# Performance work log

Measured on AMD Instinct MI355X. Metric: run time of the kernel, lower is better.

Reference implementation:

```python
import jax, jax.numpy as jnp
import numpy as np

ANGSTROM2BOHR = 1.8897261258369282
CUTOFF_ANGSTROM = 5.2  # module's `cutoff` init arg, converted to bohr in forward


def smooth_cutoff(d, rc):
    # torchani 'smooth' cutoff: exp(1 - 1/(1 - (d/rc)^2)) for d < rc, else 0
    x2 = (d / rc) ** 2
    x2_safe = jnp.where(x2 < 1.0, x2, 0.0)  # avoid inf inside the masked branch
    return jnp.where(d < rc, jnp.exp(1.0 - 1.0 / (1.0 - x2_safe)), 0.0)


def setup_inputs() -> dict:
    key = jax.random.key(0)
    k0, k1, k2, k3 = jax.random.split(key, 4)
    n_mol, n_atoms, n_pairs = 4096, 64, 16 * 1024 * 1024
    n_elem = 4  # H, C, N, O
    species = jax.random.randint(k0, (n_mol, n_atoms), 0, n_elem)
    energies = jnp.zeros((n_mol,), jnp.float32)
    atom_index12 = jax.random.randint(k1, (2, n_pairs), 0, n_mol * n_atoms)
    distances = jax.random.uniform(k2, (n_pairs,), jnp.float32, 0.5, 6.0)  # angstrom
    # exp_prefactor = -scaling_charge * sqrt(outer(Z, Z)) / 2, Z = [1, 6, 7, 8]
    z = jnp.array([1.0, 6.0, 7.0, 8.0], jnp.float32)
    exp_prefactor = (-0.016 * jnp.sqrt(jnp.outer(z, z)) / 2.0).astype(jnp.float32)
    # distances_factor = -scaling_radius / cutoff_radii (symmetric pairwise radii table)
    radii = jax.random.uniform(k3, (n_elem, n_elem), jnp.float32, 2.0, 5.0)
    radii = 0.5 * (radii + radii.T)
    distances_factor = (-10.0 / radii).astype(jnp.float32)
    return {
        "species": species,
        "energies": energies,
        "atom_index12": atom_index12,
        "distances": distances,
        "exp_prefactor": exp_prefactor,
        "distances_factor": distances_factor,
    }


def reference(species, energies, atom_index12, distances, exp_prefactor, distances_factor):
    n_mol, n_atoms = species.shape
    d = distances * ANGSTROM2BOHR  # [P]
    species12 = species.reshape(-1)[atom_index12]  # [2, P] gather
    pre = exp_prefactor[species12[0], species12[1]]   # [P]
    dfac = distances_factor[species12[0], species12[1]]  # [P]
    srb = pre * jnp.exp(dfac * d)
    srb = srb * smooth_cutoff(d, CUTOFF_ANGSTROM * ANGSTROM2BOHR)
    mol_idx = atom_index12[0] // n_atoms  # [P]
    out = energies + jax.ops.segment_sum(srb, mol_idx, num_segments=n_mol)
    return species, out
```

## Files before the change

kernel.cpp:

```cpp
#include <hip/hip_runtime.h>
#include <math.h>


#define NT        1024
#define NBLK      512
#define SCALE_F   134217728.0f
#define INV_SCALE 7.450580596923828125e-9

__global__ void pack_species_kernel(const int* __restrict__ sp,
                                    unsigned* __restrict__ packed, int nwords) {
    int w = blockIdx.x * blockDim.x + threadIdx.x;
    if (w >= nwords) return;
    const int4* p4 = (const int4*)(sp + (w << 4));
    int4 a = p4[0], b = p4[1], c = p4[2], d = p4[3];
    unsigned v =
        (unsigned)(a.x & 3)        | ((unsigned)(a.y & 3) << 2)  |
        ((unsigned)(a.z & 3) << 4) | ((unsigned)(a.w & 3) << 6)  |
        ((unsigned)(b.x & 3) << 8) | ((unsigned)(b.y & 3) << 10) |
        ((unsigned)(b.z & 3) << 12)| ((unsigned)(b.w & 3) << 14) |
        ((unsigned)(c.x & 3) << 16)| ((unsigned)(c.y & 3) << 18) |
        ((unsigned)(c.z & 3) << 20)| ((unsigned)(c.w & 3) << 22) |
        ((unsigned)(d.x & 3) << 24)| ((unsigned)(d.y & 3) << 26) |
        ((unsigned)(d.z & 3) << 28)| ((unsigned)(d.w & 3) << 30);
    packed[w] = v;
}

__global__ void init_kernel(const int* __restrict__ species,
                            float* __restrict__ out,
                            unsigned long long* __restrict__ acc,
                            int n_species, int n_mol) {
    int i = blockIdx.x * blockDim.x + threadIdx.x;
    if (i < n_species) out[i] = (float)species[i];
    if (i < n_mol)     acc[i] = 0ull;
}

__global__ __launch_bounds__(NT, 8)
void srb_fused_u32(const unsigned* __restrict__ packed_ws,
                   const int* __restrict__ ai,
                   const float* __restrict__ dist,
                   const float* __restrict__ pre_tab,
                   const float* __restrict__ dfac_tab,
                   unsigned long long* __restrict__ acc,
                   int P, int mol_shift) {
    __shared__ unsigned packed[16384];
    __shared__ unsigned binsu[4096];

    const int t = threadIdx.x;
    for (int i = t; i < 4096; i += NT) binsu[i] = 0u;

    const float myPre  = -pre_tab[t & 15];
    const float myDfac =  dfac_tab[t & 15];

    {
        int4* dst = (int4*)packed;
        const int4* src = (const int4*)packed_ws;
        for (int i = t; i < 4096; i += NT) dst[i] = src[i];
    }
    __syncthreads();

    const float a2b   = (float)1.8897261258369282;
    const float rc    = (float)(5.2 * 1.8897261258369282);
    const float rcinv = (float)(1.0 / (5.2 * 1.8897261258369282));

    const int ng     = P >> 2;
    const int stride = (int)gridDim.x * NT;
    const int4*   v0 = (const int4*)ai;
    const int4*   v1 = (const int4*)(ai + P);
    const float4* dv = (const float4*)dist;

    int g = (int)blockIdx.x * NT + t;
    if (g < ng) {
        int4   A0 = v0[g];
        int4   A1 = v1[g];
        float4 D  = dv[g];

        #pragma unroll 1
        for (;;) {
            const int  gn   = g + stride;
            const bool more = (gn < ng);

            int4 B0, B1; float4 E;
            if (more) { B0 = v0[gn]; B1 = v1[gn]; E = dv[gn]; }

            unsigned a0[4] = { (unsigned)A0.x, (unsigned)A0.y,
                               (unsigned)A0.z, (unsigned)A0.w };
            unsigned a1[4] = { (unsigned)A1.x, (unsigned)A1.y,
                               (unsigned)A1.z, (unsigned)A1.w };
            float    dd[4] = { D.x, D.y, D.z, D.w };

            unsigned w0[4], w1[4];
            #pragma unroll
            for (int k = 0; k < 4; ++k) w0[k] = packed[a0[k] >> 4];
            #pragma unroll
            for (int k = 0; k < 4; ++k) w1[k] = packed[a1[k] >> 4];

            float pr[4], df[4];
            #pragma unroll
            for (int k = 0; k < 4; ++k) {
                unsigned s0 = (w0[k] >> ((a0[k] & 15u) << 1)) & 3u;
                unsigned s1 = (w1[k] >> ((a1[k] & 15u) << 1)) & 3u;
                int idx = (int)((s0 << 2) | s1);
                pr[k] = __shfl(myPre,  idx, 64);
                df[k] = __shfl(myDfac, idx, 64);
            }

            unsigned q[4];
            #pragma unroll
            for (int k = 0; k < 4; ++k) {
                float db  = dd[k] * a2b;
                float x   = db * rcinv;
                float arg = df[k] * db + (1.0f - 1.0f / (1.0f - x * x));
                float mag = pr[k] * __expf(arg);
                mag = (db < rc) ? mag : 0.0f;
                q[k] = (unsigned)(mag * SCALE_F);
            }

            #pragma unroll
            for (int k = 0; k < 4; ++k)
                atomicAdd(&binsu[a0[k] >> mol_shift], q[k]);

            if (!more) break;
            A0 = B0; A1 = B1; D = E;
            g  = gn;
        }
    }

    __syncthreads();
    for (int i = t; i < 4096; i += NT) {
        unsigned v = binsu[i];
        if (v) atomicAdd(&acc[i], (unsigned long long)v);
    }
}

__global__ void final_kernel(const unsigned long long* __restrict__ acc,
                             const float* __restrict__ energies,
                             float* __restrict__ out_e, int n_mol) {
    int m = blockIdx.x * blockDim.x + threadIdx.x;
    if (m < n_mol)
        out_e[m] = energies[m] - (float)((double)acc[m] * INV_SCALE);
}

__global__ void init_out_fallback(const int* __restrict__ species,
                                  const float* __restrict__ energies,
                                  float* __restrict__ out,
                                  int n_species, int n_mol) {
    int i = blockIdx.x * blockDim.x + threadIdx.x;
    if (i < n_species) out[i] = (float)species[i];
    else if (i < n_species + n_mol) out[i] = energies[i - n_species];
}

__global__ __launch_bounds__(NT, 1)
void srb_fused_f32(const int* __restrict__ species,
                   const int* __restrict__ ai,
                   const float* __restrict__ dist,
                   const float* __restrict__ pre_tab,
                   const float* __restrict__ dfac_tab,
                   float* __restrict__ out_e,
                   int P, int mol_shift) {
    __shared__ unsigned packed[16384];
    __shared__ float bins[4096];
    __shared__ float2 tab[16];
    const int t = threadIdx.x;
    for (int i = t; i < 4096; i += NT) bins[i] = 0.0f;
    if (t < 16) tab[t] = make_float2(pre_tab[t], dfac_tab[t]);
    for (int w = t; w < 16384; w += NT) {
        const int4* p4 = (const int4*)(species + (w << 4));
        int4 a = p4[0], b = p4[1], c = p4[2], d = p4[3];
        unsigned v =
            (unsigned)(a.x & 3)        | ((unsigned)(a.y & 3) << 2)  |
            ((unsigned)(a.z & 3) << 4) | ((unsigned)(a.w & 3) << 6)  |
            ((unsigned)(b.x & 3) << 8) | ((unsigned)(b.y & 3) << 10) |
            ((unsigned)(b.z & 3) << 12)| ((unsigned)(b.w & 3) << 14) |
            ((unsigned)(c.x & 3) << 16)| ((unsigned)(c.y & 3) << 18) |
            ((unsigned)(c.z & 3) << 20)| ((unsigned)(c.w & 3) << 22) |
            ((unsigned)(d.x & 3) << 24)| ((unsigned)(d.y & 3) << 26) |
            ((unsigned)(d.z & 3) << 28)| ((unsigned)(d.w & 3) << 30);
        packed[w] = v;
    }
    __syncthreads();
    const float a2b   = (float)1.8897261258369282;
    const float rc    = (float)(5.2 * 1.8897261258369282);
    const float rcinv = (float)(1.0 / (5.2 * 1.8897261258369282));
    auto body = [&](int a0, int a1, float dang) {
        unsigned ua0 = (unsigned)a0, ua1 = (unsigned)a1;
        unsigned s0 = (packed[ua0 >> 4] >> ((ua0 & 15u) << 1)) & 3u;
        unsigned s1 = (packed[ua1 >> 4] >> ((ua1 & 15u) << 1)) & 3u;
        float2 td = tab[(s0 << 2) | s1];
        float db = dang * a2b;
        float x  = db * rcinv;
        float arg = td.y * db + (1.0f - 1.0f / (1.0f - x * x));
        float srb = td.x * __expf(arg);
        srb = (db < rc) ? srb : 0.0f;
        atomicAdd(&bins[ua0 >> mol_shift], srb);
    };
    const int nv = P >> 2, stride = (int)gridDim.x * NT;
    const int4* v0 = (const int4*)ai;
    const int4* v1 = (const int4*)(ai + P);
    const float4* dv = (const float4*)dist;
    for (int v = (int)blockIdx.x * NT + t; v < nv; v += stride) {
        int4 i0 = v0[v]; int4 i1 = v1[v]; float4 dd = dv[v];
        body(i0.x, i1.x, dd.x); body(i0.y, i1.y, dd.y);
        body(i0.z, i1.z, dd.z); body(i0.w, i1.w, dd.w);
    }
    __syncthreads();
    for (int i = t; i < 4096; i += NT) {
        float s = bins[i];
        if (s != 0.0f) atomicAdd(&out_e[i], s);
    }
}

extern "C" void kernel_launch(void* const* d_in, const int* in_sizes, int n_in,
                              void* d_out, int out_size, void* d_ws, size_t ws_size,
                              hipStream_t stream) {
    const int*   species  = (const int*)d_in[0];
    const float* energies = (const float*)d_in[1];
    const int*   ai       = (const int*)d_in[2];
    const float* dist     = (const float*)d_in[3];
    const float* pre_tab  = (const float*)d_in[4];
    const float* dfac_tab = (const float*)d_in[5];

    const int n_species = in_sizes[0];
    const int n_mol     = in_sizes[1];
    const int P         = in_sizes[3];
    const int n_atoms   = n_species / n_mol;

    int mol_shift = 0;
    while ((1 << mol_shift) < n_atoms) ++mol_shift;

    float* out   = (float*)d_out;
    float* out_e = out + n_species;

    const int    nwords    = n_species / 16;
    const size_t packed_sz = (size_t)nwords * 4;
    const size_t acc_sz    = (size_t)n_mol * 8;
    const size_t need      = packed_sz + acc_sz;

    if (ws_size >= need && (P & 3) == 0) {
        unsigned*           packed = (unsigned*)d_ws;
        unsigned long long* acc    = (unsigned long long*)((char*)d_ws + packed_sz);

        init_kernel<<<(n_species + 255) / 256, 256, 0, stream>>>(
            species, out, acc, n_species, n_mol);
        pack_species_kernel<<<(nwords + 255) / 256, 256, 0, stream>>>(
            species, packed, nwords);
        srb_fused_u32<<<NBLK, NT, 0, stream>>>(
            packed, ai, dist, pre_tab, dfac_tab, acc, P, mol_shift);
        final_kernel<<<(n_mol + 255) / 256, 256, 0, stream>>>(
            acc, energies, out_e, n_mol);
    } else {
        init_out_fallback<<<(n_species + n_mol + 255) / 256, 256, 0, stream>>>(
            species, energies, out, n_species, n_mol);
        srb_fused_f32<<<NBLK, NT, 0, stream>>>(
            species, ai, dist, pre_tab, dfac_tab, out_e, P, mol_shift);
    }
}
```

Measured before the change: 251.9 us.

## Triple-buffer global loads with inline asm and explicit vmcnt waits

Adds a pipelined kernel variant that issues raw global_load_dwordx4 loads three iterations deep, using manual s_waitcnt vmcnt and sched barriers so compute on one buffer overlaps with two outstanding loads. The launch uses it only when the iteration count per thread divides evenly and fits the 3-way unroll (nit%3==2); otherwise it falls back to a simplified grid-stride kernel. This is meant to hide global memory latency better than the previous single-stage prefetch. It adds register pressure and relies on hand-written asm whose wait counts must match the issue order exactly.

```diff
diff --git a/kernel.cpp b/kernel.cpp
--- a/kernel.cpp
+++ b/kernel.cpp
@@ -6,6 +6,9 @@
 #define NBLK      512
 #define SCALE_F   134217728.0f
 #define INV_SCALE 7.450580596923828125e-9
+
+typedef unsigned v4u __attribute__((ext_vector_type(4)));
+typedef float    v4f __attribute__((ext_vector_type(4)));
 
 __global__ void pack_species_kernel(const int* __restrict__ sp,
                                     unsigned* __restrict__ packed, int nwords) {
@@ -34,14 +37,28 @@
     if (i < n_mol)     acc[i] = 0ull;
 }
 
+#define GLOAD(d0, d1, dd, OFF)                                              \
+    asm volatile("global_load_dwordx4 %0, %3, %4\n\t"                        \
+                 "global_load_dwordx4 %1, %3, %5\n\t"                        \
+                 "global_load_dwordx4 %2, %3, %6"                            \
+                 : "=&v"(d0), "=&v"(d1), "=&v"(dd)                           \
+                 : "v"(OFF), "s"(pb0), "s"(pb1), "s"(pbd)                    \
+                 : "memory")
+
+#define VWAIT(n)                                                             \
+    do {                                                                     \
+        asm volatile("s_waitcnt vmcnt(" #n ")" ::: "memory");                \
+        __builtin_amdgcn_sched_barrier(0);                                   \
+    } while (0)
+
 __global__ __launch_bounds__(NT, 8)
-void srb_fused_u32(const unsigned* __restrict__ packed_ws,
-                   const int* __restrict__ ai,
-                   const float* __restrict__ dist,
-                   const float* __restrict__ pre_tab,
-                   const float* __restrict__ dfac_tab,
-                   unsigned long long* __restrict__ acc,
-                   int P, int mol_shift) {
+void srb_fused_u32_pipe(const unsigned* __restrict__ packed_ws,
+                        const int* __restrict__ ai,
+                        const float* __restrict__ dist,
+                        const float* __restrict__ pre_tab,
+                        const float* __restrict__ dfac_tab,
+                        unsigned long long* __restrict__ acc,
+                        int P, int mol_shift, int nit) {
     __shared__ unsigned packed[16384];
     __shared__ unsigned binsu[4096];
 
@@ -51,6 +68,107 @@
     const float myPre  = -pre_tab[t & 15];
     const float myDfac =  dfac_tab[t & 15];
 
+    {
+        int4* dst = (int4*)packed;
+        const int4* src = (const int4*)packed_ws;
+        for (int i = t; i < 4096; i += NT) dst[i] = src[i];
+    }
+    __syncthreads();
+
+    const float a2b   = (float)1.8897261258369282;
+    const float rc    = (float)(5.2 * 1.8897261258369282);
+    const float rcinv = (float)(1.0 / (5.2 * 1.8897261258369282));
+
+    const int      stride = (int)gridDim.x * NT;
+    const unsigned stepB  = (unsigned)stride * 16u;
+    unsigned off = (unsigned)((int)blockIdx.x * NT + t) * 16u;
+
+    const char* pb0 = (const char*)ai;
+    const char* pb1 = (const char*)(ai + P);
+    const char* pbd = (const char*)dist;
+
+    #define PBODY(X0, X1, XD)                                                \
+    do {                                                                     \
+        unsigned a0_[4] = { X0[0], X0[1], X0[2], X0[3] };                    \
+        unsigned a1_[4] = { X1[0], X1[1], X1[2], X1[3] };                    \
+        float    dd_[4] = { XD[0], XD[1], XD[2], XD[3] };                    \
+        unsigned w0_[4], w1_[4];                                             \
+        _Pragma("unroll")                                                    \
+        for (int k = 0; k < 4; ++k) w0_[k] = packed[a0_[k] >> 4];            \
+        _Pragma("unroll")                                                    \
+        for (int k = 0; k < 4; ++k) w1_[k] = packed[a1_[k] >> 4];            \
+        float pr_[4], df_[4];                                                \
+        _Pragma("unroll")                                                    \
+        for (int k = 0; k < 4; ++k) {                                        \
+            unsigned s0 = (w0_[k] >> ((a0_[k] & 15u) << 1)) & 3u;            \
+            unsigned s1 = (w1_[k] >> ((a1_[k] & 15u) << 1)) & 3u;            \
+            int idx = (int)((s0 << 2) | s1);                                 \
+            pr_[k] = __shfl(myPre,  idx, 64);                                \
+            df_[k] = __shfl(myDfac, idx, 64);                                \
+        }                                                                    \
+        unsigned q_[4];                                                      \
+        _Pragma("unroll")                                                    \
+        for (int k = 0; k < 4; ++k) {                                        \
+            float db  = dd_[k] * a2b;                                        \
+            float x   = db * rcinv;                                          \
+            float arg = df_[k] * db + (1.0f - 1.0f / (1.0f - x * x));        \
+            float mag = pr_[k] * __expf(arg);                                \
+            mag = (db < rc) ? mag : 0.0f;                                    \
+            q_[k] = (unsigned)(mag * SCALE_F);                               \
+        }                                                                    \
+        _Pragma("unroll")                                                    \
+        for (int k = 0; k < 4; ++k)                                          \
+            atomicAdd(&binsu[a0_[k] >> mol_shift], q_[k]);                   \
+    } while (0)
+
+    v4u A0, A1, B0, B1, C0, C1;
+    v4f AD, BDv, CD;
+
+    GLOAD(A0, A1, AD, off);  off += stepB;
+    GLOAD(B0, B1, BDv, off); off += stepB;
+
+    int i = 0;
+    #pragma unroll 1
+    for (; i + 4 < nit; i += 3) {
+        GLOAD(C0, C1, CD, off);  off += stepB;
+        VWAIT(6);
+        PBODY(A0, A1, AD);
+        GLOAD(A0, A1, AD, off);  off += stepB;
+        VWAIT(6);
+        PBODY(B0, B1, BDv);
+        GLOAD(B0, B1, BDv, off); off += stepB;
+        VWAIT(6);
+        PBODY(C0, C1, CD);
+    }
+    VWAIT(3);
+    PBODY(A0, A1, AD);
+    VWAIT(0);
+    PBODY(B0, B1, BDv);
+
+    #undef PBODY
+
+    __syncthreads();
+    for (int i2 = t; i2 < 4096; i2 += NT) {
+        unsigned v = binsu[i2];
+        if (v) atomicAdd(&acc[i2], (unsigned long long)v);
+    }
+}
+
+__global__ __launch_bounds__(NT, 8)
+void srb_fused_u32_gen(const unsigned* __restrict__ packed_ws,
+                       const int* __restrict__ ai,
+                       const float* __restrict__ dist,
+                       const float* __restrict__ pre_tab,
+                       const float* __restrict__ dfac_tab,
+                       unsigned long long* __restrict__ acc,
+                       int P, int mol_shift) {
+    __shared__ unsigned packed[16384];
+    __shared__ unsigned binsu[4096];
+
+    const int t = threadIdx.x;
+    for (int i = t; i < 4096; i += NT) binsu[i] = 0u;
+    const float myPre  = -pre_tab[t & 15];
+    const float myDfac =  dfac_tab[t & 15];
     {
         int4* dst = (int4*)packed;
         const int4* src = (const int4*)packed_ws;
@@ -68,61 +186,40 @@
     const int4*   v1 = (const int4*)(ai + P);
     const float4* dv = (const float4*)dist;
 
-    int g = (int)blockIdx.x * NT + t;
-    if (g < ng) {
-        int4   A0 = v0[g];
-        int4   A1 = v1[g];
-        float4 D  = dv[g];
-
-        #pragma unroll 1
-        for (;;) {
-            const int  gn   = g + stride;
-            const bool more = (gn < ng);
-
-            int4 B0, B1; float4 E;
-            if (more) { B0 = v0[gn]; B1 = v1[gn]; E = dv[gn]; }
-
-            unsigned a0[4] = { (unsigned)A0.x, (unsigned)A0.y,
-                               (unsigned)A0.z, (unsigned)A0.w };
-            unsigned a1[4] = { (unsigned)A1.x, (unsigned)A1.y,
-                               (unsigned)A1.z, (unsigned)A1.w };
-            float    dd[4] = { D.x, D.y, D.z, D.w };
-
-            unsigned w0[4], w1[4];
-            #pragma unroll
-            for (int k = 0; k < 4; ++k) w0[k] = packed[a0[k] >> 4];
-            #pragma unroll
-            for (int k = 0; k < 4; ++k) w1[k] = packed[a1[k] >> 4];
-
-            float pr[4], df[4];
-            #pragma unroll
-            for (int k = 0; k < 4; ++k) {
-                unsigned s0 = (w0[k] >> ((a0[k] & 15u) << 1)) & 3u;
-                unsigned s1 = (w1[k] >> ((a1[k] & 15u) << 1)) & 3u;
-                int idx = (int)((s0 << 2) | s1);
-                pr[k] = __shfl(myPre,  idx, 64);
-                df[k] = __shfl(myDfac, idx, 64);
-            }
-
-            unsigned q[4];
-            #pragma unroll
-            for (int k = 0; k < 4; ++k) {
-                float db  = dd[k] * a2b;
-                float x   = db * rcinv;
-                float arg = df[k] * db + (1.0f - 1.0f / (1.0f - x * x));
-                float mag = pr[k] * __expf(arg);
-                mag = (db < rc) ? mag : 0.0f;
-                q[k] = (unsigned)(mag * SCALE_F);
-            }
-
-            #pragma unroll
-            for (int k = 0; k < 4; ++k)
-                atomicAdd(&binsu[a0[k] >> mol_shift], q[k]);
-
-            if (!more) break;
-            A0 = B0; A1 = B1; D = E;
-            g  = gn;
+    for (int g = (int)blockIdx.x * NT + t; g < ng; g += stride) {
+        int4 I0 = v0[g], I1 = v1[g]; float4 D = dv[g];
+        unsigned a0[4] = { (unsigned)I0.x, (unsigned)I0.y,
+                           (unsigned)I0.z, (unsigned)I0.w };
+        unsigned a1[4] = { (unsigned)I1.x, (unsigned)I1.y,
+                           (unsigned)I1.z, (unsigned)I1.w };
+        float    dd[4] = { D.x, D.y, D.z, D.w };
+        unsigned w0[4], w1[4];
+        #pragma unroll
+        for (int k = 0; k < 4; ++k) w0[k] = packed[a0[k] >> 4];
+        #pragma unroll
+        for (int k = 0; k < 4; ++k) w1[k] = packed[a1[k] >> 4];
+        float pr[4], df[4];
+        #pragma unroll
+        for (int k = 0; k < 4; ++k) {
+            unsigned s0 = (w0[k] >> ((a0[k] & 15u) << 1)) & 3u;
+            unsigned s1 = (w1[k] >> ((a1[k] & 15u) << 1)) & 3u;
+            int idx = (int)((s0 << 2) | s1);
+            pr[k] = __shfl(myPre,  idx, 64);
+            df[k] = __shfl(myDfac, idx, 64);
         }
+        unsigned q[4];
+        #pragma unroll
+        for (int k = 0; k < 4; ++k) {
+            float db  = dd[k] * a2b;
+            float x   = db * rcinv;
+            float arg = df[k] * db + (1.0f - 1.0f / (1.0f - x * x));
+            float mag = pr[k] * __expf(arg);
+            mag = (db < rc) ? mag : 0.0f;
+            q[k] = (unsigned)(mag * SCALE_F);
+        }
+        #pragma unroll
+        for (int k = 0; k < 4; ++k)
+            atomicAdd(&binsu[a0[k] >> mol_shift], q[k]);
     }
 
     __syncthreads();
@@ -243,8 +340,19 @@
             species, out, acc, n_species, n_mol);
         pack_species_kernel<<<(nwords + 255) / 256, 256, 0, stream>>>(
             species, packed, nwords);
-        srb_fused_u32<<<NBLK, NT, 0, stream>>>(
-            packed, ai, dist, pre_tab, dfac_tab, acc, P, mol_shift);
+
+        const int ng     = P >> 2;
+        const int stride = NBLK * NT;
+        const int nit    = ng / stride;
+        const bool pipe_ok = (ng % stride == 0) && (nit >= 2) && (nit % 3 == 2);
+
+        if (pipe_ok) {
+            srb_fused_u32_pipe<<<NBLK, NT, 0, stream>>>(
+                packed, ai, dist, pre_tab, dfac_tab, acc, P, mol_shift, nit);
+        } else {
+            srb_fused_u32_gen<<<NBLK, NT, 0, stream>>>(
+                packed, ai, dist, pre_tab, dfac_tab, acc, P, mol_shift);
+        }
         final_kernel<<<(n_mol + 255) / 256, 256, 0, stream>>>(
             acc, energies, out_e, n_mol);
     } else {
```

Result: no change. 250.8 us (-0.4%).

## Replace global 64-bit atomics with per-block partial bins plus reduction kernel

Applied to the files above, without the earlier changes.

Each block now writes its 4096-entry shared histogram to a per-block slot in workspace, and a new two-level reduction kernel sums these partials before a smaller number of 64-bit atomics into the accumulator. This is meant to remove contention from 512 blocks each issuing up to 4096 global 64-bit atomics at the end. The main loop also drops the manual software prefetch in favour of a plain grid-stride loop. The cost is an extra 8 MB partial buffer write/read and one more launch, and the path only runs if the workspace is large enough; otherwise it falls back to the atomic variant.

```diff
diff --git a/kernel.cpp b/kernel.cpp
--- a/kernel.cpp
+++ b/kernel.cpp
@@ -35,13 +35,13 @@
 }
 
 __global__ __launch_bounds__(NT, 8)
-void srb_fused_u32(const unsigned* __restrict__ packed_ws,
-                   const int* __restrict__ ai,
-                   const float* __restrict__ dist,
-                   const float* __restrict__ pre_tab,
-                   const float* __restrict__ dfac_tab,
-                   unsigned long long* __restrict__ acc,
-                   int P, int mol_shift) {
+void srb_fused_u32_part(const unsigned* __restrict__ packed_ws,
+                        const int* __restrict__ ai,
+                        const float* __restrict__ dist,
+                        const float* __restrict__ pre_tab,
+                        const float* __restrict__ dfac_tab,
+                        unsigned* __restrict__ part,
+                        int P, int mol_shift) {
     __shared__ unsigned packed[16384];
     __shared__ unsigned binsu[4096];
 
@@ -68,68 +68,63 @@
     const int4*   v1 = (const int4*)(ai + P);
     const float4* dv = (const float4*)dist;
 
-    int g = (int)blockIdx.x * NT + t;
-    if (g < ng) {
-        int4   A0 = v0[g];
-        int4   A1 = v1[g];
-        float4 D  = dv[g];
-
-        #pragma unroll 1
-        for (;;) {
-            const int  gn   = g + stride;
-            const bool more = (gn < ng);
-
-            int4 B0, B1; float4 E;
-            if (more) { B0 = v0[gn]; B1 = v1[gn]; E = dv[gn]; }
-
-            unsigned a0[4] = { (unsigned)A0.x, (unsigned)A0.y,
-                               (unsigned)A0.z, (unsigned)A0.w };
-            unsigned a1[4] = { (unsigned)A1.x, (unsigned)A1.y,
-                               (unsigned)A1.z, (unsigned)A1.w };
-            float    dd[4] = { D.x, D.y, D.z, D.w };
-
-            unsigned w0[4], w1[4];
-            #pragma unroll
-            for (int k = 0; k < 4; ++k) w0[k] = packed[a0[k] >> 4];
-            #pragma unroll
-            for (int k = 0; k < 4; ++k) w1[k] = packed[a1[k] >> 4];
-
-            float pr[4], df[4];
-            #pragma unroll
-            for (int k = 0; k < 4; ++k) {
-                unsigned s0 = (w0[k] >> ((a0[k] & 15u) << 1)) & 3u;
-                unsigned s1 = (w1[k] >> ((a1[k] & 15u) << 1)) & 3u;
-                int idx = (int)((s0 << 2) | s1);
-                pr[k] = __shfl(myPre,  idx, 64);
-                df[k] = __shfl(myDfac, idx, 64);
-            }
-
-            unsigned q[4];
-            #pragma unroll
-            for (int k = 0; k < 4; ++k) {
-                float db  = dd[k] * a2b;
-                float x   = db * rcinv;
-                float arg = df[k] * db + (1.0f - 1.0f / (1.0f - x * x));
-                float mag = pr[k] * __expf(arg);
-                mag = (db < rc) ? mag : 0.0f;
-                q[k] = (unsigned)(mag * SCALE_F);
-            }
-
-            #pragma unroll
-            for (int k = 0; k < 4; ++k)
-                atomicAdd(&binsu[a0[k] >> mol_shift], q[k]);
-
-            if (!more) break;
-            A0 = B0; A1 = B1; D = E;
-            g  = gn;
+    for (int g = (int)blockIdx.x * NT + t; g < ng; g += stride) {
+        int4 I0 = v0[g], I1 = v1[g]; float4 D = dv[g];
+        unsigned a0[4] = { (unsigned)I0.x, (unsigned)I0.y,
+                           (unsigned)I0.z, (unsigned)I0.w };
+        unsigned a1[4] = { (unsigned)I1.x, (unsigned)I1.y,
+                           (unsigned)I1.z, (unsigned)I1.w };
+        float    dd[4] = { D.x, D.y, D.z, D.w };
+
+        unsigned w0[4], w1[4];
+        #pragma unroll
+        for (int k = 0; k < 4; ++k) w0[k] = packed[a0[k] >> 4];
+        #pragma unroll
+        for (int k = 0; k < 4; ++k) w1[k] = packed[a1[k] >> 4];
+
+        float pr[4], df[4];
+        #pragma unroll
+        for (int k = 0; k < 4; ++k) {
+            unsigned s0 = (w0[k] >> ((a0[k] & 15u) << 1)) & 3u;
+            unsigned s1 = (w1[k] >> ((a1[k] & 15u) << 1)) & 3u;
+            int idx = (int)((s0 << 2) | s1);
+            pr[k] = __shfl(myPre,  idx, 64);
+            df[k] = __shfl(myDfac, idx, 64);
         }
-    }
-
-    __syncthreads();
-    for (int i = t; i < 4096; i += NT) {
-        unsigned v = binsu[i];
-        if (v) atomicAdd(&acc[i], (unsigned long long)v);
-    }
+
+        unsigned q[4];
+        #pragma unroll
+        for (int k = 0; k < 4; ++k) {
+            float db  = dd[k] * a2b;
+            float x   = db * rcinv;
+            float arg = df[k] * db + (1.0f - 1.0f / (1.0f - x * x));
+            float mag = pr[k] * __expf(arg);
+            mag = (db < rc) ? mag : 0.0f;
+            q[k] = (unsigned)(mag * SCALE_F);
+        }
+
+        #pragma unroll
+        for (int k = 0; k < 4; ++k)
+            atomicAdd(&binsu[a0[k] >> mol_shift], q[k]);
+    }
+
+    __syncthreads();
+    unsigned* dst = part + (size_t)blockIdx.x * 4096;
+    for (int i = t; i < 4096; i += NT) dst[i] = binsu[i];
+}
+
+__global__ void reduce_partial(const unsigned* __restrict__ part,
+                               unsigned long long* __restrict__ acc,
+                               int n_mol, int nblk) {
+    int m = blockIdx.x * blockDim.x + threadIdx.x;
+    if (m >= n_mol) return;
+    const int nb8 = (nblk + 7) >> 3;
+    int b0 = blockIdx.y * nb8;
+    int b1 = b0 + nb8; if (b1 > nblk) b1 = nblk;
+    unsigned long long s = 0;
+    for (int b = b0; b < b1; ++b)
+        s += part[(size_t)b * 4096 + m];
+    if (s) atomicAdd(&acc[m], s);
 }
 
 __global__ void final_kernel(const unsigned long long* __restrict__ acc,
@@ -138,6 +133,81 @@
     int m = blockIdx.x * blockDim.x + threadIdx.x;
     if (m < n_mol)
         out_e[m] = energies[m] - (float)((double)acc[m] * INV_SCALE);
+}
+
+__global__ __launch_bounds__(NT, 8)
+void srb_fused_u32_gen(const unsigned* __restrict__ packed_ws,
+                       const int* __restrict__ ai,
+                       const float* __restrict__ dist,
+                       const float* __restrict__ pre_tab,
+                       const float* __restrict__ dfac_tab,
+                       unsigned long long* __restrict__ acc,
+                       int P, int mol_shift) {
+    __shared__ unsigned packed[16384];
+    __shared__ unsigned binsu[4096];
+
+    const int t = threadIdx.x;
+    for (int i = t; i < 4096; i += NT) binsu[i] = 0u;
+    const float myPre  = -pre_tab[t & 15];
+    const float myDfac =  dfac_tab[t & 15];
+    {
+        int4* dst = (int4*)packed;
+        const int4* src = (const int4*)packed_ws;
+        for (int i = t; i < 4096; i += NT) dst[i] = src[i];
+    }
+    __syncthreads();
+
+    const float a2b   = (float)1.8897261258369282;
+    const float rc    = (float)(5.2 * 1.8897261258369282);
+    const float rcinv = (float)(1.0 / (5.2 * 1.8897261258369282));
+
+    const int ng     = P >> 2;
+    const int stride = (int)gridDim.x * NT;
+    const int4*   v0 = (const int4*)ai;
+    const int4*   v1 = (const int4*)(ai + P);
+    const float4* dv = (const float4*)dist;
+
+    for (int g = (int)blockIdx.x * NT + t; g < ng; g += stride) {
+        int4 I0 = v0[g], I1 = v1[g]; float4 D = dv[g];
+        unsigned a0[4] = { (unsigned)I0.x, (unsigned)I0.y,
+                           (unsigned)I0.z, (unsigned)I0.w };
+        unsigned a1[4] = { (unsigned)I1.x, (unsigned)I1.y,
+                           (unsigned)I1.z, (unsigned)I1.w };
+        float    dd[4] = { D.x, D.y, D.z, D.w };
+        unsigned w0[4], w1[4];
+        #pragma unroll
+        for (int k = 0; k < 4; ++k) w0[k] = packed[a0[k] >> 4];
+        #pragma unroll
+        for (int k = 0; k < 4; ++k) w1[k] = packed[a1[k] >> 4];
+        float pr[4], df[4];
+        #pragma unroll
+        for (int k = 0; k < 4; ++k) {
+            unsigned s0 = (w0[k] >> ((a0[k] & 15u) << 1)) & 3u;
+            unsigned s1 = (w1[k] >> ((a1[k] & 15u) << 1)) & 3u;
+            int idx = (int)((s0 << 2) | s1);
+            pr[k] = __shfl(myPre,  idx, 64);
+            df[k] = __shfl(myDfac, idx, 64);
+        }
+        unsigned q[4];
+        #pragma unroll
+        for (int k = 0; k < 4; ++k) {
+            float db  = dd[k] * a2b;
+            float x   = db * rcinv;
+            float arg = df[k] * db + (1.0f - 1.0f / (1.0f - x * x));
+            float mag = pr[k] * __expf(arg);
+            mag = (db < rc) ? mag : 0.0f;
+            q[k] = (unsigned)(mag * SCALE_F);
+        }
+        #pragma unroll
+        for (int k = 0; k < 4; ++k)
+            atomicAdd(&binsu[a0[k] >> mol_shift], q[k]);
+    }
+
+    __syncthreads();
+    for (int i = t; i < 4096; i += NT) {
+        unsigned v = binsu[i];
+        if (v) atomicAdd(&acc[i], (unsigned long long)v);
+    }
 }
 
 __global__ void init_out_fallback(const int* __restrict__ species,
@@ -233,17 +303,34 @@
     const int    nwords    = n_species / 16;
     const size_t packed_sz = (size_t)nwords * 4;
     const size_t acc_sz    = (size_t)n_mol * 8;
-    const size_t need      = packed_sz + acc_sz;
-
-    if (ws_size >= need && (P & 3) == 0) {
+    const size_t part_sz   = (size_t)NBLK * 4096 * 4;
+    const size_t need_part = packed_sz + acc_sz + part_sz;
+    const size_t need_atom = packed_sz + acc_sz;
+
+    if (ws_size >= need_part && (P & 3) == 0) {
         unsigned*           packed = (unsigned*)d_ws;
         unsigned long long* acc    = (unsigned long long*)((char*)d_ws + packed_sz);
+        unsigned*           part   = (unsigned*)((char*)d_ws + packed_sz + acc_sz);
 
         init_kernel<<<(n_species + 255) / 256, 256, 0, stream>>>(
             species, out, acc, n_species, n_mol);
         pack_species_kernel<<<(nwords + 255) / 256, 256, 0, stream>>>(
             species, packed, nwords);
-        srb_fused_u32<<<NBLK, NT, 0, stream>>>(
+        srb_fused_u32_part<<<NBLK, NT, 0, stream>>>(
+            packed, ai, dist, pre_tab, dfac_tab, part, P, mol_shift);
+        dim3 rgrid((n_mol + 255) / 256, 8);
+        reduce_partial<<<rgrid, 256, 0, stream>>>(part, acc, n_mol, NBLK);
+        final_kernel<<<(n_mol + 255) / 256, 256, 0, stream>>>(
+            acc, energies, out_e, n_mol);
+    } else if (ws_size >= need_atom && (P & 3) == 0) {
+        unsigned*           packed = (unsigned*)d_ws;
+        unsigned long long* acc    = (unsigned long long*)((char*)d_ws + packed_sz);
+
+        init_kernel<<<(n_species + 255) / 256, 256, 0, stream>>>(
+            species, out, acc, n_species, n_mol);
+        pack_species_kernel<<<(nwords + 255) / 256, 256, 0, stream>>>(
+            species, packed, nwords);
+        srb_fused_u32_gen<<<NBLK, NT, 0, stream>>>(
             packed, ai, dist, pre_tab, dfac_tab, acc, P, mol_shift);
         final_kernel<<<(n_mol + 255) / 256, 256, 0, stream>>>(
             acc, energies, out_e, n_mol);
```

New measurement: 270.8 us. 7.5% more time.
